# Kernel optimization log

Measured on AMD Instinct MI355X. Metric: run time of the kernel, lower is better.

The kernel has to match this reference:

```python
import jax, jax.numpy as jnp
import numpy as np

N, E, D, K, NCONV = 50000, 800000, 64, 3, 6


def setup_inputs() -> dict:
    key = jax.random.key(0)
    ks = jax.random.split(key, 6)
    X = jax.random.normal(ks[0], (N, D), jnp.float32)
    edge_index = jax.random.randint(ks[1], (2, E), 0, N, dtype=jnp.int64)
    edge_weight = jax.random.uniform(ks[2], (E,), jnp.float32)
    H = jax.random.normal(ks[3], (N, D), jnp.float32)
    lambda_max = jnp.ones((1,), jnp.float32) * 2.0  # typical sym-normalized Laplacian bound
    conv_w = jax.random.normal(ks[4], (NCONV, K, D, D), jnp.float32) / np.sqrt(D)
    conv_b = jnp.zeros((NCONV, D), jnp.float32)
    return {"X": X, "edge_index": edge_index, "edge_weight": edge_weight,
            "H": H, "lambda_max": lambda_max, "conv_w": conv_w, "conv_b": conv_b}


def reference(X, edge_index, edge_weight, H, lambda_max, conv_w, conv_b):
    src, dst = edge_index[0], edge_index[1]
    # symmetric normalization: norm_e = w_e / sqrt(deg_src * deg_dst)
    deg = jax.ops.segment_sum(edge_weight, src, num_segments=N)
    dinv = jnp.where(deg > 0, deg ** -0.5, 0.0)
    norm = edge_weight * dinv[src] * dinv[dst]  # [E]
    lam = lambda_max.reshape(())
    c = 2.0 / lam

    def a_prop(v):  # A_norm @ v via scatter-add over edges, [N,D]
        return jax.ops.segment_sum(norm[:, None] * v[src], dst, num_segments=N)

    def l_hat(v):  # (2/lam)(I - A_norm) v - v
        return (c - 1.0) * v - c * a_prop(v)

    def cheb(v, w, b):  # ChebConv order K: sum_k T_k(L_hat) v @ W_k + b
        tx0, tx1 = v, l_hat(v)
        out = tx0 @ w[0] + tx1 @ w[1]
        for k in range(2, K):
            tx2 = 2.0 * l_hat(tx1) - tx0
            out = out + tx2 @ w[k]
            tx0, tx1 = tx1, tx2
        return out + b

    Z = jax.nn.sigmoid(cheb(X, conv_w[0], conv_b[0]) + cheb(H, conv_w[1], conv_b[1]))
    R = jax.nn.sigmoid(cheb(X, conv_w[2], conv_b[2]) + cheb(H, conv_w[3], conv_b[3]))
    H_tilde = jnp.tanh(cheb(X, conv_w[4], conv_b[4]) + cheb(H * R, conv_w[5], conv_b[5]))
    return Z * H_tilde + (1.0 - Z) * H
```

## Files before the change

kernel.cpp:

```cpp
#include <hip/hip_runtime.h>
#include <cstdint>
#include <cstddef>

typedef unsigned int u32;
typedef unsigned short u16;
typedef unsigned long long u64;

#define D 64
#define NCH 512
#define CAP 5120

typedef __attribute__((ext_vector_type(8))) short bf16x8;
typedef __attribute__((ext_vector_type(4))) float f32x4;

static __device__ __forceinline__ float sigmoidf_(float x) {
    return 1.f / (1.f + __expf(-x));
}
static __device__ __forceinline__ u16 f2bf(float x) {
    u32 u = __float_as_uint(x);
    return (u16)((u + 0x7fffu + ((u >> 16) & 1u)) >> 16);
}
static __device__ __forceinline__ u32 packbf2(float a, float b) {
    return (u32)f2bf(a) | ((u32)f2bf(b) << 16);
}
static __device__ __forceinline__ float bflo(u32 u) { return __uint_as_float(u << 16); }
static __device__ __forceinline__ float bfhi(u32 u) { return __uint_as_float(u & 0xffff0000u); }


__global__ void init_kernel(u32* cur_d, u32* cur_s) {
    int t = threadIdx.x;
    cur_d[t] = (u32)(t * CAP);
    cur_s[t] = (u32)(t * CAP);
}

__global__ __launch_bounds__(256) void coarse_kernel(
    const int* __restrict__ src, const int* __restrict__ dst, const float* __restrict__ w,
    u32* cur_d, u32* cur_s,
    u64* __restrict__ slab_d, u32* __restrict__ slab_s,
    int E, int CE) {
    __shared__ u32 hd[256], hs[256], cd[256], cs[256];
    int t = threadIdx.x, c = blockIdx.x;
    hd[t] = 0; hs[t] = 0;
    __syncthreads();
    int e0 = c * CE, e1 = min(E, e0 + CE);
    for (int e = e0 + t; e < e1; e += 256) {
        atomicAdd(&hd[(u32)dst[e] >> 8], 1u);
        atomicAdd(&hs[(u32)src[e] >> 8], 1u);
    }
    __syncthreads();
    cd[t] = atomicAdd(&cur_d[t], hd[t]);
    cs[t] = atomicAdd(&cur_s[t], hs[t]);
    __syncthreads();
    for (int e = e0 + t; e < e1; e += 256) {
        int s = src[e], d = dst[e];
        u32 wb = (u32)f2bf(w[e]);
        u32 pd = atomicAdd(&cd[(u32)d >> 8], 1u);
        u32 ps = atomicAdd(&cs[(u32)s >> 8], 1u);
        if (pd < (u32)(((d >> 8) + 1) * CAP))
            slab_d[pd] = (u64)((u32)s | (((u32)d & 255u) << 16)) | ((u64)wb << 32);
        if (ps < (u32)(((s >> 8) + 1) * CAP))
            slab_s[ps] = ((u32)s & 255u) | (wb << 16);
    }
}

__global__ void bprefix_kernel(const u32* __restrict__ cur_d, u32* __restrict__ bstart, int NB) {
    __shared__ int sd[256];
    int t = threadIdx.x;
    int v = (t < NB) ? min((int)cur_d[t] - t * CAP, CAP) : 0;
    sd[t] = v;
    __syncthreads();
    for (int o = 1; o < 256; o <<= 1) {
        int a = (t >= o) ? sd[t - o] : 0;
        __syncthreads();
        sd[t] += a;
        __syncthreads();
    }
    bstart[t] = (u32)(sd[t] - v);
}

__global__ __launch_bounds__(256) void fine_dst_kernel(
    const u64* __restrict__ slab, const u32* __restrict__ cur_d,
    const u32* __restrict__ bstart, u32* __restrict__ edge4,
    int* __restrict__ cnt, int* __restrict__ row_start, int N_) {
    __shared__ int h[256], sd[256], cur[256];
    int b = blockIdx.x, t = threadIdx.x;
    int m = min((int)cur_d[b] - b * CAP, CAP);
    const u64* rp = slab + (size_t)b * CAP;
    h[t] = 0;
    __syncthreads();
    for (int i = t; i < m; i += 256) atomicAdd(&h[(int)((rp[i] >> 16) & 255u)], 1);
    __syncthreads();
    int v = h[t];
    sd[t] = v;
    __syncthreads();
    for (int o = 1; o < 256; o <<= 1) {
        int a = (t >= o) ? sd[t - o] : 0;
        __syncthreads();
        sd[t] += a;
        __syncthreads();
    }
    int excl = sd[t] - v;
    cur[t] = excl;
    int bs = (int)bstart[b];
    int node = (b << 8) + t;
    if (node < N_) { cnt[node] = v; row_start[node] = bs + excl; }
    __syncthreads();
    for (int i = t; i < m; i += 256) {
        u64 r = rp[i];
        int f = (int)((r >> 16) & 255u);
        int p = atomicAdd(&cur[f], 1);
        edge4[bs + p] = (u32)(r & 0xffffu) | ((u32)(r >> 32) << 16);
    }
}

__global__ __launch_bounds__(256) void fine_deg_kernel(
    const u32* __restrict__ slab_s, const u32* __restrict__ cur_s,
    float* __restrict__ dinv, int N_) {
    __shared__ float dg[256];
    int b = blockIdx.x, t = threadIdx.x;
    int m = min((int)cur_s[b] - b * CAP, CAP);
    const u32* rp = slab_s + (size_t)b * CAP;
    dg[t] = 0.f;
    __syncthreads();
    for (int i = t; i < m; i += 256) {
        u32 r = rp[i];
        atomicAdd(&dg[r & 255u], __uint_as_float(r & 0xffff0000u));
    }
    __syncthreads();
    int node = (b << 8) + t;
    if (node < N_) dinv[node] = (dg[t] > 0.f) ? rsqrtf(dg[t]) : 0.f;
}


__global__ void xh2_kernel(const float* __restrict__ X, const float* __restrict__ H,
                           const float* __restrict__ dinv,
                           u32* __restrict__ XH_u, u32* __restrict__ XH_t, int total) {
    int i = blockIdx.x * blockDim.x + threadIdx.x;
    if (i >= total) return;
    int nn = i >> 6, l = i & 63;
    const float* sp = (l < 32 ? X : H) + (size_t)nn * 64 + ((2 * l) & 63);
    float2 v = *(const float2*)sp;
    float dv = dinv[nn];
    XH_t[i] = packbf2(v.x, v.y);
    XH_u[i] = packbf2(v.x * dv, v.y * dv);
}

__global__ __launch_bounds__(256) void wt_kernel(const float* __restrict__ w, u32* __restrict__ WT) {
    __shared__ float s[64][68];
    int g = blockIdx.x, t = threadIdx.x;
    const float* wp = w + (size_t)g * 4096;
    for (int i = t; i < 1024; i += 256) {
        int k = i >> 4, c4 = (i & 15) * 4;
        *(float4*)&s[k][c4] = *(const float4*)&wp[k * 64 + c4];
    }
    __syncthreads();
    for (int i = t; i < 2048; i += 256) {
        int uk = i & 31, n = i >> 5;
        WT[(size_t)g * 2048 + n * 32 + uk] = packbf2(s[2 * uk][n], s[2 * uk + 1][n]);
    }
}


__global__ __launch_bounds__(256) void lhat128_kernel(
    const u32* __restrict__ vu, const u32* __restrict__ vt, const u32* __restrict__ w0t,
    u32* __restrict__ out_t, u32* __restrict__ out_u,
    const int* __restrict__ rs, const int* __restrict__ cnt, const float* __restrict__ dinv,
    const u32* __restrict__ edges, const float* __restrict__ lam_ptr, int n) {
    int node = (blockIdx.x * blockDim.x + threadIdx.x) >> 6;
    if (node >= n) return;
    int l = threadIdx.x & 63;
    int g = l >> 4, f = l & 15;
    int e0 = rs[node], end = e0 + cnt[node];
    float acc[8];
#pragma unroll
    for (int j = 0; j < 8; j++) acc[j] = 0.f;

    int base = e0;
    for (; base + 16 <= end; base += 16) {
        u32 r0 = edges[base + g];
        u32 r1 = edges[base + 4 + g];
        u32 r2 = edges[base + 8 + g];
        u32 r3 = edges[base + 12 + g];
        const uint4 q0 = *(const uint4*)(vu + (size_t)(r0 & 0xffffu) * 64 + 4 * f);
        const uint4 q1 = *(const uint4*)(vu + (size_t)(r1 & 0xffffu) * 64 + 4 * f);
        const uint4 q2 = *(const uint4*)(vu + (size_t)(r2 & 0xffffu) * 64 + 4 * f);
        const uint4 q3 = *(const uint4*)(vu + (size_t)(r3 & 0xffffu) * 64 + 4 * f);
        float n0 = __uint_as_float(r0 & 0xffff0000u);
        float n1 = __uint_as_float(r1 & 0xffff0000u);
        float n2 = __uint_as_float(r2 & 0xffff0000u);
        float n3 = __uint_as_float(r3 & 0xffff0000u);
        acc[0] += n0 * bflo(q0.x); acc[1] += n0 * bfhi(q0.x);
        acc[2] += n0 * bflo(q0.y); acc[3] += n0 * bfhi(q0.y);
        acc[4] += n0 * bflo(q0.z); acc[5] += n0 * bfhi(q0.z);
        acc[6] += n0 * bflo(q0.w); acc[7] += n0 * bfhi(q0.w);
        acc[0] += n1 * bflo(q1.x); acc[1] += n1 * bfhi(q1.x);
        acc[2] += n1 * bflo(q1.y); acc[3] += n1 * bfhi(q1.y);
        acc[4] += n1 * bflo(q1.z); acc[5] += n1 * bfhi(q1.z);
        acc[6] += n1 * bflo(q1.w); acc[7] += n1 * bfhi(q1.w);
        acc[0] += n2 * bflo(q2.x); acc[1] += n2 * bfhi(q2.x);
        acc[2] += n2 * bflo(q2.y); acc[3] += n2 * bfhi(q2.y);
        acc[4] += n2 * bflo(q2.z); acc[5] += n2 * bfhi(q2.z);
        acc[6] += n2 * bflo(q2.w); acc[7] += n2 * bfhi(q2.w);
        acc[0] += n3 * bflo(q3.x); acc[1] += n3 * bfhi(q3.x);
        acc[2] += n3 * bflo(q3.y); acc[3] += n3 * bfhi(q3.y);
        acc[4] += n3 * bflo(q3.z); acc[5] += n3 * bfhi(q3.z);
        acc[6] += n3 * bflo(q3.w); acc[7] += n3 * bfhi(q3.w);
    }
    for (; base < end; base += 4) {
        int ei = base + g;
        u32 r0 = (ei < end) ? edges[ei] : 0u;
        const uint4 q0 = *(const uint4*)(vu + (size_t)(r0 & 0xffffu) * 64 + 4 * f);
        float n0 = __uint_as_float(r0 & 0xffff0000u);
        acc[0] += n0 * bflo(q0.x); acc[1] += n0 * bfhi(q0.x);
        acc[2] += n0 * bflo(q0.y); acc[3] += n0 * bfhi(q0.y);
        acc[4] += n0 * bflo(q0.z); acc[5] += n0 * bfhi(q0.z);
        acc[6] += n0 * bflo(q0.w); acc[7] += n0 * bfhi(q0.w);
    }
#pragma unroll
    for (int m = 16; m <= 32; m <<= 1)
#pragma unroll
        for (int j = 0; j < 8; j++) acc[j] += __shfl_xor(acc[j], m);

    const uint4 sv = *(const uint4*)(vt + (size_t)node * 64 + 4 * f);
    float self[8];
    self[0] = bflo(sv.x); self[1] = bfhi(sv.x);
    self[2] = bflo(sv.y); self[3] = bfhi(sv.y);
    self[4] = bflo(sv.z); self[5] = bfhi(sv.z);
    self[6] = bflo(sv.w); self[7] = bfhi(sv.w);
    float c = 2.f / lam_ptr[0];
    float dv = dinv[node];
    float rx[8];
#pragma unroll
    for (int j = 0; j < 8; j++) rx[j] = (c - 1.f) * self[j] - (c * dv) * acc[j];
    if (w0t) {
        const uint4 wv4 = *(const uint4*)(w0t + (size_t)node * 64 + 4 * f);
        rx[0] = 2.f * rx[0] - bflo(wv4.x); rx[1] = 2.f * rx[1] - bfhi(wv4.x);
        rx[2] = 2.f * rx[2] - bflo(wv4.y); rx[3] = 2.f * rx[3] - bfhi(wv4.y);
        rx[4] = 2.f * rx[4] - bflo(wv4.z); rx[5] = 2.f * rx[5] - bfhi(wv4.z);
        rx[6] = 2.f * rx[6] - bflo(wv4.w); rx[7] = 2.f * rx[7] - bfhi(wv4.w);
    }
    if (l < 16) {
        uint4 o;
        o.x = packbf2(rx[0], rx[1]); o.y = packbf2(rx[2], rx[3]);
        o.z = packbf2(rx[4], rx[5]); o.w = packbf2(rx[6], rx[7]);
        *(uint4*)(out_t + (size_t)node * 64 + 4 * f) = o;
        if (out_u) {
            uint4 ou;
            ou.x = packbf2(rx[0] * dv, rx[1] * dv); ou.y = packbf2(rx[2] * dv, rx[3] * dv);
            ou.z = packbf2(rx[4] * dv, rx[5] * dv); ou.w = packbf2(rx[6] * dv, rx[7] * dv);
            *(uint4*)(out_u + (size_t)node * 64 + 4 * f) = ou;
        }
    }
}

__global__ __launch_bounds__(256) void lhat64_kernel(
    const u32* __restrict__ vu, const u32* __restrict__ vt, const u32* __restrict__ w0t,
    u32* __restrict__ out_t, u32* __restrict__ out_u,
    const int* __restrict__ rs, const int* __restrict__ cnt, const float* __restrict__ dinv,
    const u32* __restrict__ edges, const float* __restrict__ lam_ptr, int n) {
    int node = (blockIdx.x * blockDim.x + threadIdx.x) >> 6;
    if (node >= n) return;
    int l = threadIdx.x & 63;
    int g = l >> 3, f = l & 7;
    int e0 = rs[node], end = e0 + cnt[node];
    float acc[8];
#pragma unroll
    for (int j = 0; j < 8; j++) acc[j] = 0.f;

    int base = e0;
    for (; base + 16 <= end; base += 16) {
        u32 r0 = edges[base + g];
        u32 r1 = edges[base + 8 + g];
        const uint4 q0 = *(const uint4*)(vu + (size_t)(r0 & 0xffffu) * 32 + 4 * f);
        const uint4 q1 = *(const uint4*)(vu + (size_t)(r1 & 0xffffu) * 32 + 4 * f);
        float n0 = __uint_as_float(r0 & 0xffff0000u);
        float n1 = __uint_as_float(r1 & 0xffff0000u);
        acc[0] += n0 * bflo(q0.x); acc[1] += n0 * bfhi(q0.x);
        acc[2] += n0 * bflo(q0.y); acc[3] += n0 * bfhi(q0.y);
        acc[4] += n0 * bflo(q0.z); acc[5] += n0 * bfhi(q0.z);
        acc[6] += n0 * bflo(q0.w); acc[7] += n0 * bfhi(q0.w);
        acc[0] += n1 * bflo(q1.x); acc[1] += n1 * bfhi(q1.x);
        acc[2] += n1 * bflo(q1.y); acc[3] += n1 * bfhi(q1.y);
        acc[4] += n1 * bflo(q1.z); acc[5] += n1 * bfhi(q1.z);
        acc[6] += n1 * bflo(q1.w); acc[7] += n1 * bfhi(q1.w);
    }
    for (; base < end; base += 8) {
        int ei = base + g;
        u32 r0 = (ei < end) ? edges[ei] : 0u;
        const uint4 q0 = *(const uint4*)(vu + (size_t)(r0 & 0xffffu) * 32 + 4 * f);
        float n0 = __uint_as_float(r0 & 0xffff0000u);
        acc[0] += n0 * bflo(q0.x); acc[1] += n0 * bfhi(q0.x);
        acc[2] += n0 * bflo(q0.y); acc[3] += n0 * bfhi(q0.y);
        acc[4] += n0 * bflo(q0.z); acc[5] += n0 * bfhi(q0.z);
        acc[6] += n0 * bflo(q0.w); acc[7] += n0 * bfhi(q0.w);
    }
#pragma unroll
    for (int m = 8; m <= 32; m <<= 1)
#pragma unroll
        for (int j = 0; j < 8; j++) acc[j] += __shfl_xor(acc[j], m);

    const uint4 sv = *(const uint4*)(vt + (size_t)node * 32 + 4 * f);
    float self[8];
    self[0] = bflo(sv.x); self[1] = bfhi(sv.x);
    self[2] = bflo(sv.y); self[3] = bfhi(sv.y);
    self[4] = bflo(sv.z); self[5] = bfhi(sv.z);
    self[6] = bflo(sv.w); self[7] = bfhi(sv.w);
    float c = 2.f / lam_ptr[0];
    float dv = dinv[node];
    float rx[8];
#pragma unroll
    for (int j = 0; j < 8; j++) rx[j] = (c - 1.f) * self[j] - (c * dv) * acc[j];
    if (w0t) {
        const uint4 wv4 = *(const uint4*)(w0t + (size_t)node * 32 + 4 * f);
        rx[0] = 2.f * rx[0] - bflo(wv4.x); rx[1] = 2.f * rx[1] - bfhi(wv4.x);
        rx[2] = 2.f * rx[2] - bflo(wv4.y); rx[3] = 2.f * rx[3] - bfhi(wv4.y);
        rx[4] = 2.f * rx[4] - bflo(wv4.z); rx[5] = 2.f * rx[5] - bfhi(wv4.z);
        rx[6] = 2.f * rx[6] - bflo(wv4.w); rx[7] = 2.f * rx[7] - bfhi(wv4.w);
    }
    if (l < 8) {
        uint4 o;
        o.x = packbf2(rx[0], rx[1]); o.y = packbf2(rx[2], rx[3]);
        o.z = packbf2(rx[4], rx[5]); o.w = packbf2(rx[6], rx[7]);
        *(uint4*)(out_t + (size_t)node * 32 + 4 * f) = o;
        if (out_u) {
            uint4 ou;
            ou.x = packbf2(rx[0] * dv, rx[1] * dv); ou.y = packbf2(rx[2] * dv, rx[3] * dv);
            ou.z = packbf2(rx[4] * dv, rx[5] * dv); ou.w = packbf2(rx[6] * dv, rx[7] * dv);
            *(uint4*)(out_u + (size_t)node * 32 + 4 * f) = ou;
        }
    }
}

__global__ __launch_bounds__(256) void gemm_gate_kernel(
    const u32* __restrict__ A0, const u32* __restrict__ A1, const u32* __restrict__ A2,
    const u32* __restrict__ WT, const float* __restrict__ convb,
    const float* __restrict__ Hf, const float* __restrict__ dinv,
    float* __restrict__ Zb, float* __restrict__ Sh,
    u16* __restrict__ HR_t, u16* __restrict__ HR_u, int n) {
    __shared__ u32 Ws[64 * 36];
    int t = threadIdx.x;
    int wv = t >> 6, l = t & 63;
    int q = l >> 4, ml = l & 15;
    int R = blockIdx.x * 64 + wv * 16;
    int ar = R + ml; if (ar >= n) ar = n - 1;

    f32x4 S[3][4];
#pragma unroll
    for (int tg = 0; tg < 3; tg++)
#pragma unroll
        for (int ni = 0; ni < 4; ni++) S[tg][ni] = (f32x4){0.f, 0.f, 0.f, 0.f};

    for (int kt = 0; kt < 3; kt++) {
        const u32* Ap = (kt == 0) ? A0 : ((kt == 1) ? A1 : A2);
        const u32* ap = Ap + (size_t)ar * 64 + q * 4;
        bf16x8 af[2][2];
        af[0][0] = *(const bf16x8*)(ap +  0);
        af[1][0] = *(const bf16x8*)(ap + 16);
        af[0][1] = *(const bf16x8*)(ap + 32);
        af[1][1] = *(const bf16x8*)(ap + 48);
#pragma unroll
        for (int cg = 0; cg < 5; cg++) {
            int hf = cg & 1, tg = cg >> 1;
            const u32* Wp = WT + (size_t)(cg * 3 + kt) * 2048;
            __syncthreads();
            {
                int i0 = t * 4, i1 = i0 + 1024;
                uint4 w0 = *(const uint4*)(Wp + i0);
                uint4 w1 = *(const uint4*)(Wp + i1);
                *(uint4*)&Ws[(i0 >> 5) * 36 + (i0 & 31)] = w0;
                *(uint4*)&Ws[(i1 >> 5) * 36 + (i1 & 31)] = w1;
            }
            __syncthreads();
#pragma unroll
            for (int h = 0; h < 2; h++) {
                bf16x8 bw[4];
#pragma unroll
                for (int ni = 0; ni < 4; ni++)
                    bw[ni] = *(const bf16x8*)&Ws[(ni * 16 + ml) * 36 + q * 4 + h * 16];
#pragma unroll
                for (int ni = 0; ni < 4; ni++)
                    S[tg][ni] = __builtin_amdgcn_mfma_f32_16x16x32_bf16(
                        af[h][hf], bw[ni], S[tg][ni], 0, 0, 0);
            }
        }
    }
#pragma unroll
    for (int ni = 0; ni < 4; ni++) {
        int col = ni * 16 + ml;
        float bz = convb[col] + convb[64 + col];
        float br = convb[128 + col] + convb[192 + col];
#pragma unroll
        for (int reg = 0; reg < 4; reg++) {
            int row = R + q * 4 + reg;
            if (row < n) {
                size_t o = (size_t)row * 64 + col;
                float z = sigmoidf_(S[0][ni][reg] + bz);
                float r = sigmoidf_(S[1][ni][reg] + br);
                float hr = Hf[o] * r;
                float dv = dinv[row];
                Zb[o] = z;
                Sh[o] = S[2][ni][reg];
                HR_t[o] = f2bf(hr);
                HR_u[o] = f2bf(hr * dv);
            }
        }
    }
}

__global__ __launch_bounds__(256) void gemm_final_kernel(
    const u32* __restrict__ A0, const u32* __restrict__ A1, const u32* __restrict__ A2,
    const u32* __restrict__ WT, const float* __restrict__ convb,
    const float* __restrict__ Zb, const float* __restrict__ Sh, const float* __restrict__ Hf,
    float* __restrict__ outp, int n) {
    __shared__ u32 Ws[64 * 36];
    int t = threadIdx.x;
    int wv = t >> 6, l = t & 63;
    int q = l >> 4, ml = l & 15;
    int R = blockIdx.x * 64 + wv * 16;
    int ar = R + ml; if (ar >= n) ar = n - 1;

    f32x4 S[4];
#pragma unroll
    for (int ni = 0; ni < 4; ni++) S[ni] = (f32x4){0.f, 0.f, 0.f, 0.f};

    for (int kt = 0; kt < 3; kt++) {
        const u32* Ap = (kt == 0) ? A0 : ((kt == 1) ? A1 : A2);
        const u32* ap = Ap + (size_t)ar * 32 + q * 4;
        bf16x8 af[2];
        af[0] = *(const bf16x8*)(ap +  0);
        af[1] = *(const bf16x8*)(ap + 16);
        const u32* Wp = WT + (size_t)(15 + kt) * 2048;
        __syncthreads();
        {
            int i0 = t * 4, i1 = i0 + 1024;
            uint4 w0 = *(const uint4*)(Wp + i0);
            uint4 w1 = *(const uint4*)(Wp + i1);
            *(uint4*)&Ws[(i0 >> 5) * 36 + (i0 & 31)] = w0;
            *(uint4*)&Ws[(i1 >> 5) * 36 + (i1 & 31)] = w1;
        }
        __syncthreads();
#pragma unroll
        for (int h = 0; h < 2; h++) {
            bf16x8 bw[4];
#pragma unroll
            for (int ni = 0; ni < 4; ni++)
                bw[ni] = *(const bf16x8*)&Ws[(ni * 16 + ml) * 36 + q * 4 + h * 16];
#pragma unroll
            for (int ni = 0; ni < 4; ni++)
                S[ni] = __builtin_amdgcn_mfma_f32_16x16x32_bf16(af[h], bw[ni], S[ni], 0, 0, 0);
        }
    }
#pragma unroll
    for (int ni = 0; ni < 4; ni++) {
        int col = ni * 16 + ml;
        float bh = convb[256 + col] + convb[320 + col];
#pragma unroll
        for (int reg = 0; reg < 4; reg++) {
            int row = R + q * 4 + reg;
            if (row < n) {
                size_t o = (size_t)row * 64 + col;
                float z = Zb[o];
                float ht = tanhf(S[ni][reg] + Sh[o] + bh);
                outp[o] = z * ht + (1.f - z) * Hf[o];
            }
        }
    }
}


extern "C" void kernel_launch(void* const* d_in, const int* in_sizes, int n_in,
                              void* d_out, int out_size, void* d_ws, size_t ws_size,
                              hipStream_t stream) {
    const float* X     = (const float*)d_in[0];
    const int*   ei    = (const int*)d_in[1];
    const float* ew    = (const float*)d_in[2];
    const float* H     = (const float*)d_in[3];
    const float* lam   = (const float*)d_in[4];
    const float* convw = (const float*)d_in[5];
    const float* convb = (const float*)d_in[6];
    float* out = (float*)d_out;

    const int N = in_sizes[0] / D;
    const int E = in_sizes[2];
    const int* src = ei;
    const int* dst = ei + E;

    const int NB = (N + 255) >> 8;
    const int CE = (E + NCH - 1) / NCH;

    char* p = (char*)d_ws;
    auto alloc = [&](size_t bytes) {
        void* r = (void*)p;
        p += (bytes + 255) & ~(size_t)255;
        return r;
    };
    float* Zb   = (float*)alloc((size_t)N * 64 * 4);
    float* Sh   = (float*)alloc((size_t)N * 64 * 4);
    u32* XH_u = (u32*)alloc((size_t)N * 64 * 4);
    u32* XH_t = (u32*)alloc((size_t)N * 64 * 4);
    u32* T1_u = (u32*)alloc((size_t)N * 64 * 4);
    u32* T1_t = (u32*)alloc((size_t)N * 64 * 4);
    u32* T2_t = (u32*)alloc((size_t)N * 64 * 4);
    u16* HR_u = (u16*)alloc((size_t)N * 64 * 2);
    u16* HR_t = (u16*)alloc((size_t)N * 64 * 2);
    u16* U1_u = (u16*)alloc((size_t)N * 64 * 2);
    u16* U1_t = (u16*)alloc((size_t)N * 64 * 2);
    u16* U2_t = (u16*)alloc((size_t)N * 64 * 2);
    u32* edge4 = (u32*)alloc((size_t)E * 4);
    u64* slab_d = (u64*)alloc((size_t)NB * CAP * 8);
    u32* slab_s = (u32*)alloc((size_t)NB * CAP * 4);
    u32* cur_d  = (u32*)alloc(256 * 4);
    u32* cur_s  = (u32*)alloc(256 * 4);
    u32* bstart = (u32*)alloc(256 * 4);
    int* cnt       = (int*)alloc((size_t)N * 4);
    int* row_start = (int*)alloc((size_t)N * 4);
    float* dinv    = (float*)alloc((size_t)N * 4);
    u32* WT = (u32*)alloc((size_t)18 * 2048 * 4);

    const int BLK = 256;
    const int gND  = (N * D + BLK - 1) / BLK;
    const int gWav = gND;
    const int gx64 = (N + 63) / 64;

    init_kernel<<<1, 256, 0, stream>>>(cur_d, cur_s);
    coarse_kernel<<<NCH, BLK, 0, stream>>>(src, dst, ew, cur_d, cur_s, slab_d, slab_s, E, CE);
    bprefix_kernel<<<1, 256, 0, stream>>>(cur_d, bstart, NB);
    fine_dst_kernel<<<NB, BLK, 0, stream>>>(slab_d, cur_d, bstart, edge4, cnt, row_start, N);
    fine_deg_kernel<<<NB, BLK, 0, stream>>>(slab_s, cur_s, dinv, N);

    wt_kernel<<<18, BLK, 0, stream>>>(convw, WT);
    xh2_kernel<<<gND, BLK, 0, stream>>>(X, H, dinv, XH_u, XH_t, N * D);

    lhat128_kernel<<<gWav, BLK, 0, stream>>>(XH_u, XH_t, nullptr, T1_t, T1_u,
                                             row_start, cnt, dinv, edge4, lam, N);
    lhat128_kernel<<<gWav, BLK, 0, stream>>>(T1_u, T1_t, XH_t, T2_t, nullptr,
                                             row_start, cnt, dinv, edge4, lam, N);

    gemm_gate_kernel<<<gx64, BLK, 0, stream>>>(XH_t, T1_t, T2_t, WT, convb, H, dinv,
                                               Zb, Sh, HR_t, HR_u, N);

    lhat64_kernel<<<gWav, BLK, 0, stream>>>((const u32*)HR_u, (const u32*)HR_t, nullptr,
                                            (u32*)U1_t, (u32*)U1_u,
                                            row_start, cnt, dinv, edge4, lam, N);
    lhat64_kernel<<<gWav, BLK, 0, stream>>>((const u32*)U1_u, (const u32*)U1_t, (const u32*)HR_t,
                                            (u32*)U2_t, nullptr,
                                            row_start, cnt, dinv, edge4, lam, N);

    gemm_final_kernel<<<gx64, BLK, 0, stream>>>((const u32*)HR_t, (const u32*)U1_t, (const u32*)U2_t,
                                                WT, convb, Zb, Sh, H, out, N);
}
```

Baseline: 312.2 us.

## Split Laplacian propagation by feature slice across blocks to shrink gathered row width

The propagation kernels now give each block one feature slice, 16 bf16 pairs (64 bytes) wide, out of 4 slices for the 128-wide pass or 2 for the 64-wide pass. Within a wave, 16 edges are processed in parallel with 4 lanes per edge, instead of 4 or 8 edges. Adjacent blocks handle different slices of the same nodes, so more edges are in flight per wave and the gathered rows are spread over more blocks. In exchange, edge indices are read once per slice, the shuffle reduction gains extra steps, and each gather fetches a narrower 64-byte segment.

Result: slower. 444.8 us (+42.5%).

```diff
diff --git a/kernel.cpp b/kernel.cpp
--- a/kernel.cpp
+++ b/kernel.cpp
@@ -160,119 +160,28 @@
     }
 }
 
-
-__global__ __launch_bounds__(256) void lhat128_kernel(
+__global__ __launch_bounds__(256) void lhat128s_kernel(
     const u32* __restrict__ vu, const u32* __restrict__ vt, const u32* __restrict__ w0t,
     u32* __restrict__ out_t, u32* __restrict__ out_u,
     const int* __restrict__ rs, const int* __restrict__ cnt, const float* __restrict__ dinv,
     const u32* __restrict__ edges, const float* __restrict__ lam_ptr, int n) {
-    int node = (blockIdx.x * blockDim.x + threadIdx.x) >> 6;
+    int slice = blockIdx.x & 3;
+    int node = (blockIdx.x >> 2) * 4 + (threadIdx.x >> 6);
     if (node >= n) return;
     int l = threadIdx.x & 63;
-    int g = l >> 4, f = l & 15;
+    int g = l >> 2, f = l & 3;
+    int col = slice * 16 + 4 * f;
     int e0 = rs[node], end = e0 + cnt[node];
     float acc[8];
 #pragma unroll
     for (int j = 0; j < 8; j++) acc[j] = 0.f;
 
     int base = e0;
-    for (; base + 16 <= end; base += 16) {
+    for (; base + 32 <= end; base += 32) {
         u32 r0 = edges[base + g];
-        u32 r1 = edges[base + 4 + g];
-        u32 r2 = edges[base + 8 + g];
-        u32 r3 = edges[base + 12 + g];
-        const uint4 q0 = *(const uint4*)(vu + (size_t)(r0 & 0xffffu) * 64 + 4 * f);
-        const uint4 q1 = *(const uint4*)(vu + (size_t)(r1 & 0xffffu) * 64 + 4 * f);
-        const uint4 q2 = *(const uint4*)(vu + (size_t)(r2 & 0xffffu) * 64 + 4 * f);
-        const uint4 q3 = *(const uint4*)(vu + (size_t)(r3 & 0xffffu) * 64 + 4 * f);
-        float n0 = __uint_as_float(r0 & 0xffff0000u);
-        float n1 = __uint_as_float(r1 & 0xffff0000u);
-        float n2 = __uint_as_float(r2 & 0xffff0000u);
-        float n3 = __uint_as_float(r3 & 0xffff0000u);
-        acc[0] += n0 * bflo(q0.x); acc[1] += n0 * bfhi(q0.x);
-        acc[2] += n0 * bflo(q0.y); acc[3] += n0 * bfhi(q0.y);
-        acc[4] += n0 * bflo(q0.z); acc[5] += n0 * bfhi(q0.z);
-        acc[6] += n0 * bflo(q0.w); acc[7] += n0 * bfhi(q0.w);
-        acc[0] += n1 * bflo(q1.x); acc[1] += n1 * bfhi(q1.x);
-        acc[2] += n1 * bflo(q1.y); acc[3] += n1 * bfhi(q1.y);
-        acc[4] += n1 * bflo(q1.z); acc[5] += n1 * bfhi(q1.z);
-        acc[6] += n1 * bflo(q1.w); acc[7] += n1 * bfhi(q1.w);
-        acc[0] += n2 * bflo(q2.x); acc[1] += n2 * bfhi(q2.x);
-        acc[2] += n2 * bflo(q2.y); acc[3] += n2 * bfhi(q2.y);
-        acc[4] += n2 * bflo(q2.z); acc[5] += n2 * bfhi(q2.z);
-        acc[6] += n2 * bflo(q2.w); acc[7] += n2 * bfhi(q2.w);
-        acc[0] += n3 * bflo(q3.x); acc[1] += n3 * bfhi(q3.x);
-        acc[2] += n3 * bflo(q3.y); acc[3] += n3 * bfhi(q3.y);
-        acc[4] += n3 * bflo(q3.z); acc[5] += n3 * bfhi(q3.z);
-        acc[6] += n3 * bflo(q3.w); acc[7] += n3 * bfhi(q3.w);
-    }
-    for (; base < end; base += 4) {
-        int ei = base + g;
-        u32 r0 = (ei < end) ? edges[ei] : 0u;
-        const uint4 q0 = *(const uint4*)(vu + (size_t)(r0 & 0xffffu) * 64 + 4 * f);
-        float n0 = __uint_as_float(r0 & 0xffff0000u);
-        acc[0] += n0 * bflo(q0.x); acc[1] += n0 * bfhi(q0.x);
-        acc[2] += n0 * bflo(q0.y); acc[3] += n0 * bfhi(q0.y);
-        acc[4] += n0 * bflo(q0.z); acc[5] += n0 * bfhi(q0.z);
-        acc[6] += n0 * bflo(q0.w); acc[7] += n0 * bfhi(q0.w);
-    }
-#pragma unroll
-    for (int m = 16; m <= 32; m <<= 1)
-#pragma unroll
-        for (int j = 0; j < 8; j++) acc[j] += __shfl_xor(acc[j], m);
-
-    const uint4 sv = *(const uint4*)(vt + (size_t)node * 64 + 4 * f);
-    float self[8];
-    self[0] = bflo(sv.x); self[1] = bfhi(sv.x);
-    self[2] = bflo(sv.y); self[3] = bfhi(sv.y);
-    self[4] = bflo(sv.z); self[5] = bfhi(sv.z);
-    self[6] = bflo(sv.w); self[7] = bfhi(sv.w);
-    float c = 2.f / lam_ptr[0];
-    float dv = dinv[node];
-    float rx[8];
-#pragma unroll
-    for (int j = 0; j < 8; j++) rx[j] = (c - 1.f) * self[j] - (c * dv) * acc[j];
-    if (w0t) {
-        const uint4 wv4 = *(const uint4*)(w0t + (size_t)node * 64 + 4 * f);
-        rx[0] = 2.f * rx[0] - bflo(wv4.x); rx[1] = 2.f * rx[1] - bfhi(wv4.x);
-        rx[2] = 2.f * rx[2] - bflo(wv4.y); rx[3] = 2.f * rx[3] - bfhi(wv4.y);
-        rx[4] = 2.f * rx[4] - bflo(wv4.z); rx[5] = 2.f * rx[5] - bfhi(wv4.z);
-        rx[6] = 2.f * rx[6] - bflo(wv4.w); rx[7] = 2.f * rx[7] - bfhi(wv4.w);
-    }
-    if (l < 16) {
-        uint4 o;
-        o.x = packbf2(rx[0], rx[1]); o.y = packbf2(rx[2], rx[3]);
-        o.z = packbf2(rx[4], rx[5]); o.w = packbf2(rx[6], rx[7]);
-        *(uint4*)(out_t + (size_t)node * 64 + 4 * f) = o;
-        if (out_u) {
-            uint4 ou;
-            ou.x = packbf2(rx[0] * dv, rx[1] * dv); ou.y = packbf2(rx[2] * dv, rx[3] * dv);
-            ou.z = packbf2(rx[4] * dv, rx[5] * dv); ou.w = packbf2(rx[6] * dv, rx[7] * dv);
-            *(uint4*)(out_u + (size_t)node * 64 + 4 * f) = ou;
-        }
-    }
-}
-
-__global__ __launch_bounds__(256) void lhat64_kernel(
-    const u32* __restrict__ vu, const u32* __restrict__ vt, const u32* __restrict__ w0t,
-    u32* __restrict__ out_t, u32* __restrict__ out_u,
-    const int* __restrict__ rs, const int* __restrict__ cnt, const float* __restrict__ dinv,
-    const u32* __restrict__ edges, const float* __restrict__ lam_ptr, int n) {
-    int node = (blockIdx.x * blockDim.x + threadIdx.x) >> 6;
-    if (node >= n) return;
-    int l = threadIdx.x & 63;
-    int g = l >> 3, f = l & 7;
-    int e0 = rs[node], end = e0 + cnt[node];
-    float acc[8];
-#pragma unroll
-    for (int j = 0; j < 8; j++) acc[j] = 0.f;
-
-    int base = e0;
-    for (; base + 16 <= end; base += 16) {
-        u32 r0 = edges[base + g];
-        u32 r1 = edges[base + 8 + g];
-        const uint4 q0 = *(const uint4*)(vu + (size_t)(r0 & 0xffffu) * 32 + 4 * f);
-        const uint4 q1 = *(const uint4*)(vu + (size_t)(r1 & 0xffffu) * 32 + 4 * f);
+        u32 r1 = edges[base + 16 + g];
+        const uint4 q0 = *(const uint4*)(vu + (size_t)(r0 & 0xffffu) * 64 + col);
+        const uint4 q1 = *(const uint4*)(vu + (size_t)(r1 & 0xffffu) * 64 + col);
         float n0 = __uint_as_float(r0 & 0xffff0000u);
         float n1 = __uint_as_float(r1 & 0xffff0000u);
         acc[0] += n0 * bflo(q0.x); acc[1] += n0 * bfhi(q0.x);
@@ -284,10 +193,10 @@
         acc[4] += n1 * bflo(q1.z); acc[5] += n1 * bfhi(q1.z);
         acc[6] += n1 * bflo(q1.w); acc[7] += n1 * bfhi(q1.w);
     }
-    for (; base < end; base += 8) {
+    for (; base < end; base += 16) {
         int ei = base + g;
         u32 r0 = (ei < end) ? edges[ei] : 0u;
-        const uint4 q0 = *(const uint4*)(vu + (size_t)(r0 & 0xffffu) * 32 + 4 * f);
+        const uint4 q0 = *(const uint4*)(vu + (size_t)(r0 & 0xffffu) * 64 + col);
         float n0 = __uint_as_float(r0 & 0xffff0000u);
         acc[0] += n0 * bflo(q0.x); acc[1] += n0 * bfhi(q0.x);
         acc[2] += n0 * bflo(q0.y); acc[3] += n0 * bfhi(q0.y);
@@ -295,38 +204,122 @@
         acc[6] += n0 * bflo(q0.w); acc[7] += n0 * bfhi(q0.w);
     }
 #pragma unroll
-    for (int m = 8; m <= 32; m <<= 1)
+    for (int m = 4; m <= 32; m <<= 1)
 #pragma unroll
         for (int j = 0; j < 8; j++) acc[j] += __shfl_xor(acc[j], m);
 
-    const uint4 sv = *(const uint4*)(vt + (size_t)node * 32 + 4 * f);
-    float self[8];
-    self[0] = bflo(sv.x); self[1] = bfhi(sv.x);
-    self[2] = bflo(sv.y); self[3] = bfhi(sv.y);
-    self[4] = bflo(sv.z); self[5] = bfhi(sv.z);
-    self[6] = bflo(sv.w); self[7] = bfhi(sv.w);
-    float c = 2.f / lam_ptr[0];
-    float dv = dinv[node];
-    float rx[8];
-#pragma unroll
-    for (int j = 0; j < 8; j++) rx[j] = (c - 1.f) * self[j] - (c * dv) * acc[j];
-    if (w0t) {
-        const uint4 wv4 = *(const uint4*)(w0t + (size_t)node * 32 + 4 * f);
-        rx[0] = 2.f * rx[0] - bflo(wv4.x); rx[1] = 2.f * rx[1] - bfhi(wv4.x);
-        rx[2] = 2.f * rx[2] - bflo(wv4.y); rx[3] = 2.f * rx[3] - bfhi(wv4.y);
-        rx[4] = 2.f * rx[4] - bflo(wv4.z); rx[5] = 2.f * rx[5] - bfhi(wv4.z);
-        rx[6] = 2.f * rx[6] - bflo(wv4.w); rx[7] = 2.f * rx[7] - bfhi(wv4.w);
-    }
-    if (l < 8) {
+    if (l < 4) {
+        int c4 = slice * 16 + 4 * l;
+        const uint4 sv = *(const uint4*)(vt + (size_t)node * 64 + c4);
+        float c = 2.f / lam_ptr[0];
+        float dv = dinv[node];
+        float rx[8];
+        rx[0] = (c - 1.f) * bflo(sv.x) - (c * dv) * acc[0];
+        rx[1] = (c - 1.f) * bfhi(sv.x) - (c * dv) * acc[1];
+        rx[2] = (c - 1.f) * bflo(sv.y) - (c * dv) * acc[2];
+        rx[3] = (c - 1.f) * bfhi(sv.y) - (c * dv) * acc[3];
+        rx[4] = (c - 1.f) * bflo(sv.z) - (c * dv) * acc[4];
+        rx[5] = (c - 1.f) * bfhi(sv.z) - (c * dv) * acc[5];
+        rx[6] = (c - 1.f) * bflo(sv.w) - (c * dv) * acc[6];
+        rx[7] = (c - 1.f) * bfhi(sv.w) - (c * dv) * acc[7];
+        if (w0t) {
+            const uint4 wv4 = *(const uint4*)(w0t + (size_t)node * 64 + c4);
+            rx[0] = 2.f * rx[0] - bflo(wv4.x); rx[1] = 2.f * rx[1] - bfhi(wv4.x);
+            rx[2] = 2.f * rx[2] - bflo(wv4.y); rx[3] = 2.f * rx[3] - bfhi(wv4.y);
+            rx[4] = 2.f * rx[4] - bflo(wv4.z); rx[5] = 2.f * rx[5] - bfhi(wv4.z);
+            rx[6] = 2.f * rx[6] - bflo(wv4.w); rx[7] = 2.f * rx[7] - bfhi(wv4.w);
+        }
         uint4 o;
         o.x = packbf2(rx[0], rx[1]); o.y = packbf2(rx[2], rx[3]);
         o.z = packbf2(rx[4], rx[5]); o.w = packbf2(rx[6], rx[7]);
-        *(uint4*)(out_t + (size_t)node * 32 + 4 * f) = o;
+        *(uint4*)(out_t + (size_t)node * 64 + c4) = o;
         if (out_u) {
             uint4 ou;
             ou.x = packbf2(rx[0] * dv, rx[1] * dv); ou.y = packbf2(rx[2] * dv, rx[3] * dv);
             ou.z = packbf2(rx[4] * dv, rx[5] * dv); ou.w = packbf2(rx[6] * dv, rx[7] * dv);
-            *(uint4*)(out_u + (size_t)node * 32 + 4 * f) = ou;
+            *(uint4*)(out_u + (size_t)node * 64 + c4) = ou;
+        }
+    }
+}
+
+__global__ __launch_bounds__(256) void lhat64s_kernel(
+    const u32* __restrict__ vu, const u32* __restrict__ vt, const u32* __restrict__ w0t,
+    u32* __restrict__ out_t, u32* __restrict__ out_u,
+    const int* __restrict__ rs, const int* __restrict__ cnt, const float* __restrict__ dinv,
+    const u32* __restrict__ edges, const float* __restrict__ lam_ptr, int n) {
+    int slice = blockIdx.x & 1;
+    int node = (blockIdx.x >> 1) * 4 + (threadIdx.x >> 6);
+    if (node >= n) return;
+    int l = threadIdx.x & 63;
+    int g = l >> 2, f = l & 3;
+    int col = slice * 16 + 4 * f;
+    int e0 = rs[node], end = e0 + cnt[node];
+    float acc[8];
+#pragma unroll
+    for (int j = 0; j < 8; j++) acc[j] = 0.f;
+
+    int base = e0;
+    for (; base + 32 <= end; base += 32) {
+        u32 r0 = edges[base + g];
+        u32 r1 = edges[base + 16 + g];
+        const uint4 q0 = *(const uint4*)(vu + (size_t)(r0 & 0xffffu) * 32 + col);
+        const uint4 q1 = *(const uint4*)(vu + (size_t)(r1 & 0xffffu) * 32 + col);
+        float n0 = __uint_as_float(r0 & 0xffff0000u);
+        float n1 = __uint_as_float(r1 & 0xffff0000u);
+        acc[0] += n0 * bflo(q0.x); acc[1] += n0 * bfhi(q0.x);
+        acc[2] += n0 * bflo(q0.y); acc[3] += n0 * bfhi(q0.y);
+        acc[4] += n0 * bflo(q0.z); acc[5] += n0 * bfhi(q0.z);
+        acc[6] += n0 * bflo(q0.w); acc[7] += n0 * bfhi(q0.w);
+        acc[0] += n1 * bflo(q1.x); acc[1] += n1 * bfhi(q1.x);
+        acc[2] += n1 * bflo(q1.y); acc[3] += n1 * bfhi(q1.y);
+        acc[4] += n1 * bflo(q1.z); acc[5] += n1 * bfhi(q1.z);
+        acc[6] += n1 * bflo(q1.w); acc[7] += n1 * bfhi(q1.w);
+    }
+    for (; base < end; base += 16) {
+        int ei = base + g;
+        u32 r0 = (ei < end) ? edges[ei] : 0u;
+        const uint4 q0 = *(const uint4*)(vu + (size_t)(r0 & 0xffffu) * 32 + col);
+        float n0 = __uint_as_float(r0 & 0xffff0000u);
+        acc[0] += n0 * bflo(q0.x); acc[1] += n0 * bfhi(q0.x);
+        acc[2] += n0 * bflo(q0.y); acc[3] += n0 * bfhi(q0.y);
+        acc[4] += n0 * bflo(q0.z); acc[5] += n0 * bfhi(q0.z);
+        acc[6] += n0 * bflo(q0.w); acc[7] += n0 * bfhi(q0.w);
+    }
+#pragma unroll
+    for (int m = 4; m <= 32; m <<= 1)
+#pragma unroll
+        for (int j = 0; j < 8; j++) acc[j] += __shfl_xor(acc[j], m);
+
+    if (l < 4) {
+        int c4 = slice * 16 + 4 * l;
+        const uint4 sv = *(const uint4*)(vt + (size_t)node * 32 + c4);
+        float c = 2.f / lam_ptr[0];
+        float dv = dinv[node];
+        float rx[8];
+        rx[0] = (c - 1.f) * bflo(sv.x) - (c * dv) * acc[0];
+        rx[1] = (c - 1.f) * bfhi(sv.x) - (c * dv) * acc[1];
+        rx[2] = (c - 1.f) * bflo(sv.y) - (c * dv) * acc[2];
+        rx[3] = (c - 1.f) * bfhi(sv.y) - (c * dv) * acc[3];
+        rx[4] = (c - 1.f) * bflo(sv.z) - (c * dv) * acc[4];
+        rx[5] = (c - 1.f) * bfhi(sv.z) - (c * dv) * acc[5];
+        rx[6] = (c - 1.f) * bflo(sv.w) - (c * dv) * acc[6];
+        rx[7] = (c - 1.f) * bfhi(sv.w) - (c * dv) * acc[7];
+        if (w0t) {
+            const uint4 wv4 = *(const uint4*)(w0t + (size_t)node * 32 + c4);
+            rx[0] = 2.f * rx[0] - bflo(wv4.x); rx[1] = 2.f * rx[1] - bfhi(wv4.x);
+            rx[2] = 2.f * rx[2] - bflo(wv4.y); rx[3] = 2.f * rx[3] - bfhi(wv4.y);
+            rx[4] = 2.f * rx[4] - bflo(wv4.z); rx[5] = 2.f * rx[5] - bfhi(wv4.z);
+            rx[6] = 2.f * rx[6] - bflo(wv4.w); rx[7] = 2.f * rx[7] - bfhi(wv4.w);
+        }
+        uint4 o;
+        o.x = packbf2(rx[0], rx[1]); o.y = packbf2(rx[2], rx[3]);
+        o.z = packbf2(rx[4], rx[5]); o.w = packbf2(rx[6], rx[7]);
+        *(uint4*)(out_t + (size_t)node * 32 + c4) = o;
+        if (out_u) {
+            uint4 ou;
+            ou.x = packbf2(rx[0] * dv, rx[1] * dv); ou.y = packbf2(rx[2] * dv, rx[3] * dv);
+            ou.z = packbf2(rx[4] * dv, rx[5] * dv); ou.w = packbf2(rx[6] * dv, rx[7] * dv);
+            *(uint4*)(out_u + (size_t)node * 32 + c4) = ou;
         }
     }
 }
@@ -519,8 +512,8 @@
 
     const int BLK = 256;
     const int gND  = (N * D + BLK - 1) / BLK;
-    const int gWav = gND;
     const int gx64 = (N + 63) / 64;
+    const int nb4  = (N + 3) / 4;
 
     init_kernel<<<1, 256, 0, stream>>>(cur_d, cur_s);
     coarse_kernel<<<NCH, BLK, 0, stream>>>(src, dst, ew, cur_d, cur_s, slab_d, slab_s, E, CE);
@@ -531,20 +524,20 @@
     wt_kernel<<<18, BLK, 0, stream>>>(convw, WT);
     xh2_kernel<<<gND, BLK, 0, stream>>>(X, H, dinv, XH_u, XH_t, N * D);
 
-    lhat128_kernel<<<gWav, BLK, 0, stream>>>(XH_u, XH_t, nullptr, T1_t, T1_u,
-                                             row_start, cnt, dinv, edge4, lam, N);
-    lhat128_kernel<<<gWav, BLK, 0, stream>>>(T1_u, T1_t, XH_t, T2_t, nullptr,
-                                             row_start, cnt, dinv, edge4, lam, N);
+    lhat128s_kernel<<<nb4 * 4, BLK, 0, stream>>>(XH_u, XH_t, nullptr, T1_t, T1_u,
+                                                 row_start, cnt, dinv, edge4, lam, N);
+    lhat128s_kernel<<<nb4 * 4, BLK, 0, stream>>>(T1_u, T1_t, XH_t, T2_t, nullptr,
+                                                 row_start, cnt, dinv, edge4, lam, N);
 
     gemm_gate_kernel<<<gx64, BLK, 0, stream>>>(XH_t, T1_t, T2_t, WT, convb, H, dinv,
                                                Zb, Sh, HR_t, HR_u, N);
 
-    lhat64_kernel<<<gWav, BLK, 0, stream>>>((const u32*)HR_u, (const u32*)HR_t, nullptr,
-                                            (u32*)U1_t, (u32*)U1_u,
-                                            row_start, cnt, dinv, edge4, lam, N);
-    lhat64_kernel<<<gWav, BLK, 0, stream>>>((const u32*)U1_u, (const u32*)U1_t, (const u32*)HR_t,
-                                            (u32*)U2_t, nullptr,
-                                            row_start, cnt, dinv, edge4, lam, N);
+    lhat64s_kernel<<<nb4 * 2, BLK, 0, stream>>>((const u32*)HR_u, (const u32*)HR_t, nullptr,
+                                                (u32*)U1_t, (u32*)U1_u,
+                                                row_start, cnt, dinv, edge4, lam, N);
+    lhat64s_kernel<<<nb4 * 2, BLK, 0, stream>>>((const u32*)U1_u, (const u32*)U1_t, (const u32*)HR_t,
+                                                (u32*)U2_t, nullptr,
+                                                row_start, cnt, dinv, edge4, lam, N);
 
     gemm_final_kernel<<<gx64, BLK, 0, stream>>>((const u32*)HR_t, (const u32*)U1_t, (const u32*)U2_t,
                                                 WT, convb, Zb, Sh, H, out, N);
```
